# Kernel optimization log

Hardware: AMD Instinct MI355X
Metric: run time of the kernel (lower is better)

Reference implementation:

```python
import jax, jax.numpy as jnp
import numpy as np

VOCAB, EMB_DIM, HIDDEN, NUM_CLASSES = 100000, 128, 256, 20
B, S = 4096, 200


def setup_inputs() -> dict:
    key = jax.random.key(0)
    k1, k2, k3, k4, k5, k6, k7 = jax.random.split(key, 7)
    x = jax.random.randint(k1, (B, S), 0, VOCAB, dtype=jnp.int64)
    seq_lengths = jnp.maximum(jax.random.randint(k2, (B,), 0, S, dtype=jnp.int64), 1)
    emb = jax.random.normal(k3, (VOCAB, EMB_DIM), dtype=jnp.float32) * 0.02
    emb = emb.at[0].set(0.0)  # padding_idx=0
    W1 = jax.random.normal(k4, (EMB_DIM, HIDDEN), dtype=jnp.float32) * (1.0 / np.sqrt(EMB_DIM))
    b1 = jax.random.normal(k5, (HIDDEN,), dtype=jnp.float32) * 0.01
    W2 = jax.random.normal(k6, (HIDDEN, NUM_CLASSES), dtype=jnp.float32) * (1.0 / np.sqrt(HIDDEN))
    b2 = jax.random.normal(k7, (NUM_CLASSES,), dtype=jnp.float32) * 0.01
    return {"x": x, "seq_lengths": seq_lengths, "emb": emb, "W1": W1, "b1": b1, "W2": W2, "b2": b2}


def reference(x, seq_lengths, emb, W1, b1, W2, b2):
    # Embedding lookup: [B, S, D]
    e = emb[x]
    # Masked mean over first seq_lengths[i] positions (fused, no per-sample loop)
    mask = (jnp.arange(S)[None, :] < seq_lengths[:, None]).astype(e.dtype)  # [B, S]
    pooled = jnp.einsum('bsd,bs->bd', e, mask) / seq_lengths[:, None].astype(e.dtype)
    # MLP (dropout is identity in eval mode)
    hidden = jax.nn.relu(pooled @ W1 + b1)
    return hidden @ W2 + b2
```

## Files before the change

### kernel.cpp

```cpp
#include <hip/hip_runtime.h>
#include <hip/hip_bf16.h>

#define B 4096
#define S 200
#define EMB_DIM 128
#define HIDDEN 256
#define NUM_CLASSES 20
#define VOCAB 100000
#define RB 2

typedef __attribute__((ext_vector_type(8))) unsigned short ushort8;

__device__ __forceinline__ unsigned short f2bf(float f) {
    unsigned u = __float_as_uint(f);
    unsigned r = u + 0x7fffu + ((u >> 16) & 1u);
    return (unsigned short)(r >> 16);
}

__global__ __launch_bounds__(256) void convert_kernel(
    const float* __restrict__ emb,
    unsigned short* __restrict__ embh)
{
    const long i = ((long)blockIdx.x * 256 + threadIdx.x) * 8;
    const float4 a = *(const float4*)(emb + i);
    const float4 b = *(const float4*)(emb + i + 4);
    ushort8 o;
    o[0] = f2bf(a.x); o[1] = f2bf(a.y); o[2] = f2bf(a.z); o[3] = f2bf(a.w);
    o[4] = f2bf(b.x); o[5] = f2bf(b.y); o[6] = f2bf(b.z); o[7] = f2bf(b.w);
    *(ushort8*)(embh + i) = o;
}

__global__ __launch_bounds__(256) void fused_kernel(
    const int* __restrict__ x,
    const int* __restrict__ lens,
    const unsigned short* __restrict__ embh,
    const float* __restrict__ W1,
    const float* __restrict__ b1,
    const float* __restrict__ W2,
    const float* __restrict__ b2,
    float* __restrict__ out)
{
    __shared__ int   sidx[RB][256];
    __shared__ float tmp[16][16][8];
    __shared__ float P[RB][EMB_DIM];
    __shared__ float H[RB][HIDDEN];
    __shared__ float part[RB][4][NUM_CLASSES];

    const int t  = threadIdx.x;
    const int b0 = blockIdx.x * RB;

    int Ls[RB];
    #pragma unroll
    for (int r = 0; r < RB; ++r) {
        Ls[r] = lens[b0 + r];
        int v = 0;
        if (t < Ls[r]) v = x[(long)(b0 + r) * S + t];
        sidx[r][t] = v;
    }
    __syncthreads();

    const int g = t >> 4;
    const int d = t & 15;

    for (int r = 0; r < RB; ++r) {
        const int L = Ls[r];
        const int nIter = ((L + 63) & ~63) >> 6;

        float acc[4][8];
        #pragma unroll
        for (int j = 0; j < 4; ++j)
            #pragma unroll
            for (int f = 0; f < 8; ++f) acc[j][f] = 0.f;

        int cur[4], nxt[4];
        #pragma unroll
        for (int j = 0; j < 4; ++j) cur[j] = sidx[r][g + 16 * j];

        for (int it = 0; it < nIter; ++it) {
            uint4 v[4];
            #pragma unroll
            for (int j = 0; j < 4; ++j)
                v[j] = *(const uint4*)(embh + (long)cur[j] * EMB_DIM + d * 8);

            if (it + 1 < nIter) {
                const int nb = (it + 1) << 6;
                #pragma unroll
                for (int j = 0; j < 4; ++j) nxt[j] = sidx[r][nb + g + 16 * j];
            }

            #pragma unroll
            for (int j = 0; j < 4; ++j) {
                const unsigned c0 = v[j].x, c1 = v[j].y, c2 = v[j].z, c3 = v[j].w;
                acc[j][0] += __uint_as_float(c0 << 16);
                acc[j][1] += __uint_as_float(c0 & 0xffff0000u);
                acc[j][2] += __uint_as_float(c1 << 16);
                acc[j][3] += __uint_as_float(c1 & 0xffff0000u);
                acc[j][4] += __uint_as_float(c2 << 16);
                acc[j][5] += __uint_as_float(c2 & 0xffff0000u);
                acc[j][6] += __uint_as_float(c3 << 16);
                acc[j][7] += __uint_as_float(c3 & 0xffff0000u);
            }
            #pragma unroll
            for (int j = 0; j < 4; ++j) cur[j] = nxt[j];
        }

        #pragma unroll
        for (int f = 0; f < 8; ++f)
            tmp[g][d][f] = acc[0][f] + acc[1][f] + acc[2][f] + acc[3][f];
        __syncthreads();

        if (t < EMB_DIM) {
            float s = 0.f;
            #pragma unroll
            for (int gg = 0; gg < 16; ++gg) s += tmp[gg][t >> 3][t & 7];
            P[r][t] = s / (float)L;
        }
        __syncthreads();
    }

    {
        float h0a = 0.f, h0b = 0.f, h1a = 0.f, h1b = 0.f;
        for (int k = 0; k < EMB_DIM; k += 2) {
            const float wa = W1[(k)     * HIDDEN + t];
            const float wb = W1[(k + 1) * HIDDEN + t];
            h0a += P[0][k] * wa;  h0b += P[0][k + 1] * wb;
            h1a += P[1][k] * wa;  h1b += P[1][k + 1] * wb;
        }
        const float bb = b1[t];
        H[0][t] = fmaxf(h0a + h0b + bb, 0.f);
        H[1][t] = fmaxf(h1a + h1b + bb, 0.f);
    }
    __syncthreads();

    if (t < RB * 4 * NUM_CLASSES) {
        const int r  = t / (4 * NUM_CLASSES);
        const int u  = t - r * 4 * NUM_CLASSES;
        const int j  = u / NUM_CLASSES;
        const int c  = u - j * NUM_CLASSES;
        const int k0 = j * 64;
        float a = 0.f;
        for (int k = k0; k < k0 + 64; ++k)
            a += H[r][k] * W2[k * NUM_CLASSES + c];
        part[r][j][c] = a;
    }
    __syncthreads();

    if (t < RB * NUM_CLASSES) {
        const int r = t / NUM_CLASSES;
        const int c = t - r * NUM_CLASSES;
        const float a = b2[c] + part[r][0][c] + part[r][1][c]
                              + part[r][2][c] + part[r][3][c];
        out[(long)(b0 + r) * NUM_CLASSES + c] = a;
    }
}

extern "C" void kernel_launch(void* const* d_in, const int* in_sizes, int n_in,
                              void* d_out, int out_size, void* d_ws, size_t ws_size,
                              hipStream_t stream) {
    const int*   x    = (const int*)d_in[0];
    const int*   lens = (const int*)d_in[1];
    const float* emb  = (const float*)d_in[2];
    const float* W1   = (const float*)d_in[3];
    const float* b1   = (const float*)d_in[4];
    const float* W2   = (const float*)d_in[5];
    const float* b2   = (const float*)d_in[6];
    float*       out  = (float*)d_out;

    unsigned short* embh = (unsigned short*)d_ws;

    convert_kernel<<<(VOCAB * EMB_DIM) / (8 * 256), 256, 0, stream>>>(emb, embh);
    fused_kernel<<<B / RB, 256, 0, stream>>>(x, lens, embh, W1, b1, W2, b2, out);
}
```

Baseline: 126.5 us.

## Split MLP into separate batched kernel and trim gather tail loads

```diff
diff --git a/kernel.cpp b/kernel.cpp
--- a/kernel.cpp
+++ b/kernel.cpp
@@ -1,5 +1,4 @@
 #include <hip/hip_runtime.h>
-#include <hip/hip_bf16.h>
 
 #define B 4096
 #define S 200
@@ -8,6 +7,7 @@
 #define NUM_CLASSES 20
 #define VOCAB 100000
 #define RB 2
+#define MR 8
 
 typedef __attribute__((ext_vector_type(8))) unsigned short ushort8;
 
@@ -30,21 +30,14 @@
     *(ushort8*)(embh + i) = o;
 }
 
-__global__ __launch_bounds__(256) void fused_kernel(
+__global__ __launch_bounds__(256) void gather_kernel(
     const int* __restrict__ x,
     const int* __restrict__ lens,
     const unsigned short* __restrict__ embh,
-    const float* __restrict__ W1,
-    const float* __restrict__ b1,
-    const float* __restrict__ W2,
-    const float* __restrict__ b2,
-    float* __restrict__ out)
+    float* __restrict__ Pg)
 {
     __shared__ int   sidx[RB][256];
     __shared__ float tmp[16][16][8];
-    __shared__ float P[RB][EMB_DIM];
-    __shared__ float H[RB][HIDDEN];
-    __shared__ float part[RB][4][NUM_CLASSES];
 
     const int t  = threadIdx.x;
     const int b0 = blockIdx.x * RB;
@@ -63,8 +56,10 @@
     const int d = t & 15;
 
     for (int r = 0; r < RB; ++r) {
-        const int L = Ls[r];
-        const int nIter = ((L + 63) & ~63) >> 6;
+        const int L     = Ls[r];
+        const int nJ    = (L + 15) >> 4;
+        const int nFull = nJ >> 2;
+        const int tailJ = nJ & 3;
 
         float acc[4][8];
         #pragma unroll
@@ -76,17 +71,15 @@
         #pragma unroll
         for (int j = 0; j < 4; ++j) cur[j] = sidx[r][g + 16 * j];
 
-        for (int it = 0; it < nIter; ++it) {
+        for (int it = 0; it < nFull; ++it) {
             uint4 v[4];
             #pragma unroll
             for (int j = 0; j < 4; ++j)
                 v[j] = *(const uint4*)(embh + (long)cur[j] * EMB_DIM + d * 8);
 
-            if (it + 1 < nIter) {
-                const int nb = (it + 1) << 6;
-                #pragma unroll
-                for (int j = 0; j < 4; ++j) nxt[j] = sidx[r][nb + g + 16 * j];
-            }
+            const int nb = (it + 1) << 6;
+            #pragma unroll
+            for (int j = 0; j < 4; ++j) nxt[j] = sidx[r][nb + g + 16 * j];
 
             #pragma unroll
             for (int j = 0; j < 4; ++j) {
@@ -104,6 +97,27 @@
             for (int j = 0; j < 4; ++j) cur[j] = nxt[j];
         }
 
+        if (tailJ) {
+            uint4 v[4];
+            #pragma unroll
+            for (int j = 0; j < 4; ++j)
+                if (j < tailJ)
+                    v[j] = *(const uint4*)(embh + (long)cur[j] * EMB_DIM + d * 8);
+            #pragma unroll
+            for (int j = 0; j < 4; ++j)
+                if (j < tailJ) {
+                    const unsigned c0 = v[j].x, c1 = v[j].y, c2 = v[j].z, c3 = v[j].w;
+                    acc[j][0] += __uint_as_float(c0 << 16);
+                    acc[j][1] += __uint_as_float(c0 & 0xffff0000u);
+                    acc[j][2] += __uint_as_float(c1 << 16);
+                    acc[j][3] += __uint_as_float(c1 & 0xffff0000u);
+                    acc[j][4] += __uint_as_float(c2 << 16);
+                    acc[j][5] += __uint_as_float(c2 & 0xffff0000u);
+                    acc[j][6] += __uint_as_float(c3 << 16);
+                    acc[j][7] += __uint_as_float(c3 & 0xffff0000u);
+                }
+        }
+
         #pragma unroll
         for (int f = 0; f < 8; ++f)
             tmp[g][d][f] = acc[0][f] + acc[1][f] + acc[2][f] + acc[3][f];
@@ -113,44 +127,61 @@
             float s = 0.f;
             #pragma unroll
             for (int gg = 0; gg < 16; ++gg) s += tmp[gg][t >> 3][t & 7];
-            P[r][t] = s / (float)L;
+            Pg[(long)(b0 + r) * EMB_DIM + t] = s / (float)L;
         }
         __syncthreads();
     }
-
-    {
-        float h0a = 0.f, h0b = 0.f, h1a = 0.f, h1b = 0.f;
-        for (int k = 0; k < EMB_DIM; k += 2) {
-            const float wa = W1[(k)     * HIDDEN + t];
-            const float wb = W1[(k + 1) * HIDDEN + t];
-            h0a += P[0][k] * wa;  h0b += P[0][k + 1] * wb;
-            h1a += P[1][k] * wa;  h1b += P[1][k + 1] * wb;
-        }
-        const float bb = b1[t];
-        H[0][t] = fmaxf(h0a + h0b + bb, 0.f);
-        H[1][t] = fmaxf(h1a + h1b + bb, 0.f);
-    }
+}
+
+__global__ __launch_bounds__(256) void mlp_kernel(
+    const float* __restrict__ Pg,
+    const float* __restrict__ W1,
+    const float* __restrict__ b1,
+    const float* __restrict__ W2,
+    const float* __restrict__ b2,
+    float* __restrict__ out)
+{
+    __shared__ float H[MR][HIDDEN + 1];
+
+    const int  t  = threadIdx.x;
+    const long r0 = (long)blockIdx.x * MR;
+
+    float acc[MR];
+    #pragma unroll
+    for (int i = 0; i < MR; ++i) acc[i] = 0.f;
+
+    const float* Pb = Pg + r0 * EMB_DIM;
+    for (int k = 0; k < EMB_DIM; k += 4) {
+        const float w0 = W1[(k + 0) * HIDDEN + t];
+        const float w1 = W1[(k + 1) * HIDDEN + t];
+        const float w2 = W1[(k + 2) * HIDDEN + t];
+        const float w3 = W1[(k + 3) * HIDDEN + t];
+        #pragma unroll
+        for (int i = 0; i < MR; ++i) {
+            const float4 p = *(const float4*)(Pb + i * EMB_DIM + k);
+            acc[i] = fmaf(p.x, w0, acc[i]);
+            acc[i] = fmaf(p.y, w1, acc[i]);
+            acc[i] = fmaf(p.z, w2, acc[i]);
+            acc[i] = fmaf(p.w, w3, acc[i]);
+        }
+    }
+    const float bb = b1[t];
+    #pragma unroll
+    for (int i = 0; i < MR; ++i)
+        H[i][t] = fmaxf(acc[i] + bb, 0.f);
     __syncthreads();
 
-    if (t < RB * 4 * NUM_CLASSES) {
-        const int r  = t / (4 * NUM_CLASSES);
-        const int u  = t - r * 4 * NUM_CLASSES;
-        const int j  = u / NUM_CLASSES;
-        const int c  = u - j * NUM_CLASSES;
-        const int k0 = j * 64;
-        float a = 0.f;
-        for (int k = k0; k < k0 + 64; ++k)
-            a += H[r][k] * W2[k * NUM_CLASSES + c];
-        part[r][j][c] = a;
-    }
-    __syncthreads();
-
-    if (t < RB * NUM_CLASSES) {
+    if (t < MR * NUM_CLASSES) {
         const int r = t / NUM_CLASSES;
         const int c = t - r * NUM_CLASSES;
-        const float a = b2[c] + part[r][0][c] + part[r][1][c]
-                              + part[r][2][c] + part[r][3][c];
-        out[(long)(b0 + r) * NUM_CLASSES + c] = a;
+        float a0 = 0.f, a1 = 0.f, a2 = 0.f, a3 = 0.f;
+        for (int k = 0; k < HIDDEN; k += 4) {
+            a0 = fmaf(H[r][k + 0], W2[(k + 0) * NUM_CLASSES + c], a0);
+            a1 = fmaf(H[r][k + 1], W2[(k + 1) * NUM_CLASSES + c], a1);
+            a2 = fmaf(H[r][k + 2], W2[(k + 2) * NUM_CLASSES + c], a2);
+            a3 = fmaf(H[r][k + 3], W2[(k + 3) * NUM_CLASSES + c], a3);
+        }
+        out[(r0 + r) * NUM_CLASSES + c] = b2[c] + a0 + a1 + a2 + a3;
     }
 }
 
@@ -167,7 +198,9 @@
     float*       out  = (float*)d_out;
 
     unsigned short* embh = (unsigned short*)d_ws;
+    float*          Pg   = (float*)((char*)d_ws + (32l << 20));
 
     convert_kernel<<<(VOCAB * EMB_DIM) / (8 * 256), 256, 0, stream>>>(emb, embh);
-    fused_kernel<<<B / RB, 256, 0, stream>>>(x, lens, embh, W1, b1, W2, b2, out);
-}
+    gather_kernel<<<B / RB, 256, 0, stream>>>(x, lens, embh, Pg);
+    mlp_kernel<<<B / MR, 256, 0, stream>>>(Pg, W1, b1, W2, b2, out);
+}
```

After: 135.3 us. +7.0%, slower.

## Interleave both rows' embedding gathers in one loop and merge reductions

Applied to the files above, without the earlier changes.

```diff
diff --git a/kernel.cpp b/kernel.cpp
--- a/kernel.cpp
+++ b/kernel.cpp
@@ -1,5 +1,4 @@
 #include <hip/hip_runtime.h>
-#include <hip/hip_bf16.h>
 
 #define B 4096
 #define S 200
@@ -41,7 +40,7 @@
     float* __restrict__ out)
 {
     __shared__ int   sidx[RB][256];
-    __shared__ float tmp[16][16][8];
+    __shared__ float tmp[RB][16][16][8];
     __shared__ float P[RB][EMB_DIM];
     __shared__ float H[RB][HIDDEN];
     __shared__ float part[RB][4][NUM_CLASSES];
@@ -62,61 +61,76 @@
     const int g = t >> 4;
     const int d = t & 15;
 
-    for (int r = 0; r < RB; ++r) {
-        const int L = Ls[r];
-        const int nIter = ((L + 63) & ~63) >> 6;
+    const int n0   = (Ls[0] + 63) >> 6;
+    const int n1   = (Ls[1] + 63) >> 6;
+    const int nMax = n0 > n1 ? n0 : n1;
 
-        float acc[4][8];
+    float acc[RB][8];
+    #pragma unroll
+    for (int r = 0; r < RB; ++r)
         #pragma unroll
-        for (int j = 0; j < 4; ++j)
-            #pragma unroll
-            for (int f = 0; f < 8; ++f) acc[j][f] = 0.f;
+        for (int f = 0; f < 8; ++f) acc[r][f] = 0.f;
 
-        int cur[4], nxt[4];
+    int cur[RB][4], nxt[RB][4];
+    #pragma unroll
+    for (int r = 0; r < RB; ++r)
         #pragma unroll
-        for (int j = 0; j < 4; ++j) cur[j] = sidx[r][g + 16 * j];
+        for (int j = 0; j < 4; ++j) cur[r][j] = sidx[r][g + 16 * j];
 
-        for (int it = 0; it < nIter; ++it) {
-            uint4 v[4];
+    const int dof = d << 3;
+
+    for (int it = 0; it < nMax; ++it) {
+        uint4 v[RB][4];
+        #pragma unroll
+        for (int r = 0; r < RB; ++r)
             #pragma unroll
             for (int j = 0; j < 4; ++j)
-                v[j] = *(const uint4*)(embh + (long)cur[j] * EMB_DIM + d * 8);
+                v[r][j] = *(const uint4*)(embh + ((cur[r][j] << 7) + dof));
 
-            if (it + 1 < nIter) {
-                const int nb = (it + 1) << 6;
-                #pragma unroll
-                for (int j = 0; j < 4; ++j) nxt[j] = sidx[r][nb + g + 16 * j];
+        const int nb = ((it + 1) & 3) << 6;
+        #pragma unroll
+        for (int r = 0; r < RB; ++r)
+            #pragma unroll
+            for (int j = 0; j < 4; ++j) nxt[r][j] = sidx[r][nb + g + 16 * j];
+
+        #pragma unroll
+        for (int r = 0; r < RB; ++r)
+            #pragma unroll
+            for (int j = 0; j < 4; ++j) {
+                const unsigned c0 = v[r][j].x, c1 = v[r][j].y;
+                const unsigned c2 = v[r][j].z, c3 = v[r][j].w;
+                acc[r][0] += __uint_as_float(c0 << 16);
+                acc[r][1] += __uint_as_float(c0 & 0xffff0000u);
+                acc[r][2] += __uint_as_float(c1 << 16);
+                acc[r][3] += __uint_as_float(c1 & 0xffff0000u);
+                acc[r][4] += __uint_as_float(c2 << 16);
+                acc[r][5] += __uint_as_float(c2 & 0xffff0000u);
+                acc[r][6] += __uint_as_float(c3 << 16);
+                acc[r][7] += __uint_as_float(c3 & 0xffff0000u);
             }
 
+        #pragma unroll
+        for (int r = 0; r < RB; ++r)
             #pragma unroll
-            for (int j = 0; j < 4; ++j) {
-                const unsigned c0 = v[j].x, c1 = v[j].y, c2 = v[j].z, c3 = v[j].w;
-                acc[j][0] += __uint_as_float(c0 << 16);
-                acc[j][1] += __uint_as_float(c0 & 0xffff0000u);
-                acc[j][2] += __uint_as_float(c1 << 16);
-                acc[j][3] += __uint_as_float(c1 & 0xffff0000u);
-                acc[j][4] += __uint_as_float(c2 << 16);
-                acc[j][5] += __uint_as_float(c2 & 0xffff0000u);
-                acc[j][6] += __uint_as_float(c3 << 16);
-                acc[j][7] += __uint_as_float(c3 & 0xffff0000u);
-            }
-            #pragma unroll
-            for (int j = 0; j < 4; ++j) cur[j] = nxt[j];
-        }
+            for (int j = 0; j < 4; ++j) cur[r][j] = nxt[r][j];
+    }
 
+    #pragma unroll
+    for (int r = 0; r < RB; ++r)
         #pragma unroll
         for (int f = 0; f < 8; ++f)
-            tmp[g][d][f] = acc[0][f] + acc[1][f] + acc[2][f] + acc[3][f];
-        __syncthreads();
+            tmp[r][g][d][f] = acc[r][f];
+    __syncthreads();
 
-        if (t < EMB_DIM) {
-            float s = 0.f;
-            #pragma unroll
-            for (int gg = 0; gg < 16; ++gg) s += tmp[gg][t >> 3][t & 7];
-            P[r][t] = s / (float)L;
-        }
-        __syncthreads();
+    {
+        const int r   = t >> 7;
+        const int dim = t & 127;
+        float s = 0.f;
+        #pragma unroll
+        for (int gg = 0; gg < 16; ++gg) s += tmp[r][gg][dim >> 3][dim & 7];
+        P[r][dim] = s / (float)Ls[r];
     }
+    __syncthreads();
 
     {
         float h0a = 0.f, h0b = 0.f, h1a = 0.f, h1b = 0.f;
```

New measurement: 125.2 us. No clear change (-1.0%).

## Quantize embedding table to int8 with per-row scale and restructure gather

Applied to the files above, without the earlier changes.

```diff
diff --git a/kernel.cpp b/kernel.cpp
--- a/kernel.cpp
+++ b/kernel.cpp
@@ -1,5 +1,4 @@
 #include <hip/hip_runtime.h>
-#include <hip/hip_bf16.h>
 
 #define B 4096
 #define S 200
@@ -7,124 +6,127 @@
 #define HIDDEN 256
 #define NUM_CLASSES 20
 #define VOCAB 100000
-#define RB 2
 
-typedef __attribute__((ext_vector_type(8))) unsigned short ushort8;
+__global__ __launch_bounds__(256) void convert_q8(
+    const float* __restrict__ emb,
+    signed char* __restrict__ qt,
+    float* __restrict__ scl)
+{
+    const int  t    = threadIdx.x;
+    const long base = (long)blockIdx.x * 1024 + t * 4;
+    const float4 v  = *(const float4*)(emb + base);
 
-__device__ __forceinline__ unsigned short f2bf(float f) {
-    unsigned u = __float_as_uint(f);
-    unsigned r = u + 0x7fffu + ((u >> 16) & 1u);
-    return (unsigned short)(r >> 16);
+    float m = fmaxf(fmaxf(fabsf(v.x), fabsf(v.y)),
+                    fmaxf(fabsf(v.z), fabsf(v.w)));
+    #pragma unroll
+    for (int off = 1; off < 32; off <<= 1)
+        m = fmaxf(m, __shfl_xor(m, off, 64));
+
+    const float inv = m > 0.f ? 127.f / m : 0.f;
+    const int q0 = __float2int_rn(v.x * inv);
+    const int q1 = __float2int_rn(v.y * inv);
+    const int q2 = __float2int_rn(v.z * inv);
+    const int q3 = __float2int_rn(v.w * inv);
+    const unsigned pk = (q0 & 255) | ((q1 & 255) << 8)
+                      | ((q2 & 255) << 16) | ((q3 & 255) << 24);
+    *(unsigned*)(qt + base) = pk;
+
+    if ((t & 31) == 0) scl[base >> 7] = m * (1.f / 127.f);
 }
 
-__global__ __launch_bounds__(256) void convert_kernel(
-    const float* __restrict__ emb,
-    unsigned short* __restrict__ embh)
-{
-    const long i = ((long)blockIdx.x * 256 + threadIdx.x) * 8;
-    const float4 a = *(const float4*)(emb + i);
-    const float4 b = *(const float4*)(emb + i + 4);
-    ushort8 o;
-    o[0] = f2bf(a.x); o[1] = f2bf(a.y); o[2] = f2bf(a.z); o[3] = f2bf(a.w);
-    o[4] = f2bf(b.x); o[5] = f2bf(b.y); o[6] = f2bf(b.z); o[7] = f2bf(b.w);
-    *(ushort8*)(embh + i) = o;
-}
-
-__global__ __launch_bounds__(256) void fused_kernel(
+__global__ __launch_bounds__(256, 8) void fused_kernel(
     const int* __restrict__ x,
     const int* __restrict__ lens,
-    const unsigned short* __restrict__ embh,
+    const signed char* __restrict__ qt,
+    const float* __restrict__ scl,
     const float* __restrict__ W1,
     const float* __restrict__ b1,
     const float* __restrict__ W2,
     const float* __restrict__ b2,
     float* __restrict__ out)
 {
-    __shared__ int   sidx[RB][256];
-    __shared__ float tmp[16][16][8];
-    __shared__ float P[RB][EMB_DIM];
-    __shared__ float H[RB][HIDDEN];
-    __shared__ float part[RB][4][NUM_CLASSES];
+    __shared__ int   sidx[2][256];
+    __shared__ float Pp[4][EMB_DIM];
+    __shared__ float P[2][EMB_DIM];
+    __shared__ float H[2][HIDDEN];
+    __shared__ float part[2][4][NUM_CLASSES];
 
     const int t  = threadIdx.x;
-    const int b0 = blockIdx.x * RB;
+    const int b0 = blockIdx.x * 2;
 
-    int Ls[RB];
-    #pragma unroll
-    for (int r = 0; r < RB; ++r) {
-        Ls[r] = lens[b0 + r];
-        int v = 0;
-        if (t < Ls[r]) v = x[(long)(b0 + r) * S + t];
-        sidx[r][t] = v;
+    const int L0 = lens[b0];
+    const int L1 = lens[b0 + 1];
+    {
+        int v0i = 0; if (t < L0) v0i = x[(long)b0 * S + t];
+        sidx[0][t] = v0i;
+        int v1i = 0; if (t < L1) v1i = x[(long)(b0 + 1) * S + t];
+        sidx[1][t] = v1i;
     }
     __syncthreads();
 
-    const int g = t >> 4;
-    const int d = t & 15;
+    const int l    = t & 63;
+    const int wid  = t >> 6;
+    const int smp  = wid >> 1;
+    const int w    = wid & 1;
+    const int slot = l >> 3;
+    const int sub  = l & 7;
+    const int soff = sub << 4;
 
-    for (int r = 0; r < RB; ++r) {
-        const int L = Ls[r];
-        const int nIter = ((L + 63) & ~63) >> 6;
+    const int L   = smp ? L1 : L0;
+    const int nCh = __builtin_amdgcn_readfirstlane((L + 7) >> 3);
 
-        float acc[4][8];
-        #pragma unroll
-        for (int j = 0; j < 4; ++j)
-            #pragma unroll
-            for (int f = 0; f < 8; ++f) acc[j][f] = 0.f;
+    float acc[16];
+    #pragma unroll
+    for (int f = 0; f < 16; ++f) acc[f] = 0.f;
 
-        int cur[4], nxt[4];
-        #pragma unroll
-        for (int j = 0; j < 4; ++j) cur[j] = sidx[r][g + 16 * j];
+    int  idx0 = sidx[smp][(w << 3) + slot];
+    uint4 v0  = *(const uint4*)(qt + (((long)idx0 << 7) + soff));
+    float s0  = scl[idx0];
 
-        for (int it = 0; it < nIter; ++it) {
-            uint4 v[4];
-            #pragma unroll
-            for (int j = 0; j < 4; ++j)
-                v[j] = *(const uint4*)(embh + (long)cur[j] * EMB_DIM + d * 8);
-
-            if (it + 1 < nIter) {
-                const int nb = (it + 1) << 6;
-                #pragma unroll
-                for (int j = 0; j < 4; ++j) nxt[j] = sidx[r][nb + g + 16 * j];
-            }
-
-            #pragma unroll
-            for (int j = 0; j < 4; ++j) {
-                const unsigned c0 = v[j].x, c1 = v[j].y, c2 = v[j].z, c3 = v[j].w;
-                acc[j][0] += __uint_as_float(c0 << 16);
-                acc[j][1] += __uint_as_float(c0 & 0xffff0000u);
-                acc[j][2] += __uint_as_float(c1 << 16);
-                acc[j][3] += __uint_as_float(c1 & 0xffff0000u);
-                acc[j][4] += __uint_as_float(c2 << 16);
-                acc[j][5] += __uint_as_float(c2 & 0xffff0000u);
-                acc[j][6] += __uint_as_float(c3 << 16);
-                acc[j][7] += __uint_as_float(c3 & 0xffff0000u);
-            }
-            #pragma unroll
-            for (int j = 0; j < 4; ++j) cur[j] = nxt[j];
-        }
+    for (int c = w; c < nCh; c += 2) {
+        const int   idxN = sidx[smp][((c + 2) << 3) + slot];
+        const uint4 vN   = *(const uint4*)(qt + (((long)idxN << 7) + soff));
+        const float sN   = scl[idxN];
 
         #pragma unroll
-        for (int f = 0; f < 8; ++f)
-            tmp[g][d][f] = acc[0][f] + acc[1][f] + acc[2][f] + acc[3][f];
-        __syncthreads();
+        for (int q = 0; q < 4; ++q) {
+            const unsigned cc = q == 0 ? v0.x : q == 1 ? v0.y : q == 2 ? v0.z : v0.w;
+            acc[q * 4 + 0] = fmaf(s0, (float)((int)(cc << 24) >> 24), acc[q * 4 + 0]);
+            acc[q * 4 + 1] = fmaf(s0, (float)((int)(cc << 16) >> 24), acc[q * 4 + 1]);
+            acc[q * 4 + 2] = fmaf(s0, (float)((int)(cc <<  8) >> 24), acc[q * 4 + 2]);
+            acc[q * 4 + 3] = fmaf(s0, (float)((int)(cc      ) >> 24), acc[q * 4 + 3]);
+        }
+        v0 = vN; s0 = sN; idx0 = idxN;
+    }
 
-        if (t < EMB_DIM) {
-            float s = 0.f;
-            #pragma unroll
-            for (int gg = 0; gg < 16; ++gg) s += tmp[gg][t >> 3][t & 7];
-            P[r][t] = s / (float)L;
-        }
-        __syncthreads();
+    #pragma unroll
+    for (int f = 0; f < 16; ++f) {
+        acc[f] += __shfl_xor(acc[f],  8, 64);
+        acc[f] += __shfl_xor(acc[f], 16, 64);
+        acc[f] += __shfl_xor(acc[f], 32, 64);
     }
+    if (slot == 0) {
+        #pragma unroll
+        for (int f = 0; f < 16; ++f)
+            Pp[wid][(sub << 4) + f] = acc[f];
+    }
+    __syncthreads();
+
+    {
+        const int   s2  = t >> 7;
+        const int   dim = t & 127;
+        const float Lf  = (float)(s2 ? L1 : L0);
+        P[s2][dim] = (Pp[2 * s2][dim] + Pp[2 * s2 + 1][dim]) / Lf;
+    }
+    __syncthreads();
 
     {
         float h0a = 0.f, h0b = 0.f, h1a = 0.f, h1b = 0.f;
         for (int k = 0; k < EMB_DIM; k += 2) {
             const float wa = W1[(k)     * HIDDEN + t];
             const float wb = W1[(k + 1) * HIDDEN + t];
-            h0a += P[0][k] * wa;  h0b += P[0][k + 1] * wb;
-            h1a += P[1][k] * wa;  h1b += P[1][k + 1] * wb;
+            h0a = fmaf(P[0][k],     wa, h0a);  h0b = fmaf(P[0][k + 1], wb, h0b);
+            h1a = fmaf(P[1][k],     wa, h1a);  h1b = fmaf(P[1][k + 1], wb, h1b);
         }
         const float bb = b1[t];
         H[0][t] = fmaxf(h0a + h0b + bb, 0.f);
@@ -132,7 +134,7 @@
     }
     __syncthreads();
 
-    if (t < RB * 4 * NUM_CLASSES) {
+    if (t < 2 * 4 * NUM_CLASSES) {
         const int r  = t / (4 * NUM_CLASSES);
         const int u  = t - r * 4 * NUM_CLASSES;
         const int j  = u / NUM_CLASSES;
@@ -140,17 +142,17 @@
         const int k0 = j * 64;
         float a = 0.f;
         for (int k = k0; k < k0 + 64; ++k)
-            a += H[r][k] * W2[k * NUM_CLASSES + c];
+            a = fmaf(H[r][k], W2[k * NUM_CLASSES + c], a);
         part[r][j][c] = a;
     }
     __syncthreads();
 
-    if (t < RB * NUM_CLASSES) {
+    if (t < 2 * NUM_CLASSES) {
         const int r = t / NUM_CLASSES;
         const int c = t - r * NUM_CLASSES;
-        const float a = b2[c] + part[r][0][c] + part[r][1][c]
-                              + part[r][2][c] + part[r][3][c];
-        out[(long)(b0 + r) * NUM_CLASSES + c] = a;
+        out[(long)(b0 + r) * NUM_CLASSES + c] =
+            b2[c] + part[r][0][c] + part[r][1][c]
+                  + part[r][2][c] + part[r][3][c];
     }
 }
 
@@ -166,8 +168,9 @@
     const float* b2   = (const float*)d_in[6];
     float*       out  = (float*)d_out;
 
-    unsigned short* embh = (unsigned short*)d_ws;
+    signed char* qt  = (signed char*)d_ws;
+    float*       scl = (float*)((char*)d_ws + (16l << 20));
 
-    convert_kernel<<<(VOCAB * EMB_DIM) / (8 * 256), 256, 0, stream>>>(emb, embh);
-    fused_kernel<<<B / RB, 256, 0, stream>>>(x, lens, embh, W1, b1, W2, b2, out);
+    convert_q8<<<(VOCAB * EMB_DIM) / (4 * 256), 256, 0, stream>>>(emb, qt, scl);
+    fused_kernel<<<B / 2, 256, 0, stream>>>(x, lens, qt, scl, W1, b1, W2, b2, out);
 }
```

New measurement: 120.5 us. -4.7%, faster.
